# Performance work log

Hardware: AMD Instinct MI355X
Metric: run time of the kernel (lower is better)

## Reference

```python
import jax, jax.numpy as jnp
import numpy as np

N = 100000
E = 3200000
D_IN = 128
D_H = 128
K = 3


def setup_inputs() -> dict:
    key = jax.random.key(0)
    ks = jax.random.split(key, 8)
    x = jax.random.normal(ks[0], (N, D_IN), dtype=jnp.float32)
    src = jax.random.randint(ks[1], (E,), 0, N, dtype=jnp.int32)
    dst = jax.random.randint(ks[2], (E,), 0, N, dtype=jnp.int32)
    s = 1.0 / np.sqrt(D_H)
    W1 = jax.random.normal(ks[3], (D_IN, D_H), dtype=jnp.float32) * s
    b1 = jnp.zeros((D_H,), jnp.float32)
    W2 = jax.random.normal(ks[4], (D_H, D_H), dtype=jnp.float32) * s
    b2 = jnp.zeros((D_H,), jnp.float32)
    Wf1 = jax.random.normal(ks[5], (D_H, D_H), dtype=jnp.float32) * s
    bf1 = jnp.zeros((D_H,), jnp.float32)
    Wf2 = jax.random.normal(ks[6], (D_H, 1), dtype=jnp.float32) * s
    bf2 = jnp.zeros((1,), jnp.float32)
    return {"x": x, "src": src, "dst": dst, "W1": W1, "b1": b1, "W2": W2,
            "b2": b2, "Wf1": Wf1, "bf1": bf1, "Wf2": Wf2, "bf2": bf2}


def _sg_propagate(h, src, dst, norm, k):
    # DGL SGConv: k hops of h <- D^{-1/2} A D^{-1/2} h (in-degree norm, clamp>=1)
    for _ in range(k):
        h = h * norm                                   # [N, d]
        h = jax.ops.segment_sum(h[src], dst, num_segments=N)  # SpMM hop
        h = h * norm
    return h


def reference(x, src, dst, W1, b1, W2, b2, Wf1, bf1, Wf2, bf2):
    deg = jax.ops.segment_sum(jnp.ones((E,), jnp.float32), dst, num_segments=N)
    norm = jnp.clip(deg, 1.0, None) ** -0.5            # [N]
    norm = norm[:, None]
    # conv_1: SGConv(k=3) -> linear -> ReLU
    h = _sg_propagate(x, src, dst, norm, K)
    h = jax.nn.relu(h @ W1 + b1)
    # conv_2
    h = _sg_propagate(h, src, dst, norm, K)
    h = jax.nn.relu(h @ W2 + b2)
    # dgl.mean_nodes over the single graph -> [1, D_H]
    hg = jnp.mean(h, axis=0, keepdims=True)
    h = jax.nn.relu(hg @ Wf1 + bf1)
    out = jax.nn.relu(h @ Wf2 + bf2)
    return jax.nn.sigmoid(out)                         # [1, 1]
```

## Files before the change

kernel.cpp:

```cpp
#include <hip/hip_runtime.h>
#include <hip/hip_fp16.h>
#include <math.h>

#define NN 100000
#define EE 3200000
#define D 128
#define NB 391
#define NBLK2 1024
#define ECH2 (EE / NBLK2)
#define NSTRIP (NN / 32)

#define SCALE_R 6.0f
#define SCALE_G 512.0f

typedef _Float16 half8 __attribute__((ext_vector_type(8)));
typedef float floatx16 __attribute__((ext_vector_type(16)));
typedef float v2f __attribute__((ext_vector_type(2)));

__global__ __launch_bounds__(256) void block_hist(const int* __restrict__ dst,
                                                  int* __restrict__ bh) {
    __shared__ int hist[NB];
    for (int i = threadIdx.x; i < NB; i += 256) hist[i] = 0;
    __syncthreads();
    int e0 = blockIdx.x * ECH2;
    for (int e = e0 + threadIdx.x; e < e0 + ECH2; e += 256)
        atomicAdd(&hist[dst[e] >> 8], 1);
    __syncthreads();
    for (int i = threadIdx.x; i < NB; i += 256)
        bh[i * NBLK2 + blockIdx.x] = hist[i];
}

__global__ __launch_bounds__(256) void bin_scan(int* __restrict__ bh,
                                                int* __restrict__ bintot) {
    __shared__ int ts[256];
    int i = blockIdx.x;
    int t = threadIdx.x;
    int4 v = ((int4*)(bh + i * NBLK2))[t];
    int s = v.x + v.y + v.z + v.w;
    ts[t] = s;
    __syncthreads();
    for (int off = 1; off < 256; off <<= 1) {
        int x = (t >= off) ? ts[t - off] : 0;
        __syncthreads();
        ts[t] += x;
        __syncthreads();
    }
    int run = ts[t] - s;
    int4 o;
    o.x = run; o.y = run + v.x; o.z = o.y + v.y; o.w = o.z + v.z;
    ((int4*)(bh + i * NBLK2))[t] = o;
    if (t == 255) bintot[i] = ts[255];
}

__global__ __launch_bounds__(512) void tiny_scan(const int* __restrict__ bintot,
                                                 int* __restrict__ coff) {
    __shared__ int s[512];
    int t = threadIdx.x;
    int v = (t < NB) ? bintot[t] : 0;
    s[t] = v;
    __syncthreads();
    for (int off = 1; off < 512; off <<= 1) {
        int x = (t >= off) ? s[t - off] : 0;
        __syncthreads();
        s[t] += x;
        __syncthreads();
    }
    int excl = s[t] - v;
    if (t <= NB) coff[t] = excl;
}

__global__ __launch_bounds__(256) void scatter2(const int* __restrict__ src,
                                                const int* __restrict__ dst,
                                                const int* __restrict__ bh,
                                                const int* __restrict__ coff,
                                                int2* __restrict__ ebuf) {
    __shared__ int base[NB];
    int b = blockIdx.x;
    for (int i = threadIdx.x; i < NB; i += 256)
        base[i] = coff[i] + bh[i * NBLK2 + b];
    __syncthreads();
    int e0 = b * ECH2;
    for (int e = e0 + threadIdx.x; e < e0 + ECH2; e += 256) {
        int d = dst[e];
        int pos = atomicAdd(&base[d >> 8], 1);
        ebuf[pos] = make_int2(src[e], d);
    }
}

__global__ __launch_bounds__(256) void fine_sort(const int2* __restrict__ ebuf,
                                                 const int* __restrict__ coarse_off,
                                                 int* __restrict__ rowptr,
                                                 float* __restrict__ norm,
                                                 int* __restrict__ csr) {
    __shared__ int cnt[256];
    __shared__ int sbuf[256];
    int b = blockIdx.x;
    int t = threadIdx.x;
    int e0 = coarse_off[b], e1 = coarse_off[b + 1];
    int n0 = b << 8;
    cnt[t] = 0;
    __syncthreads();
    for (int e = e0 + t; e < e1; e += 256)
        atomicAdd(&cnt[ebuf[e].y & 255], 1);
    __syncthreads();
    int myc = cnt[t];
    sbuf[t] = myc;
    __syncthreads();
    for (int off = 1; off < 256; off <<= 1) {
        int x = (t >= off) ? sbuf[t - off] : 0;
        __syncthreads();
        sbuf[t] += x;
        __syncthreads();
    }
    int excl = sbuf[t] - myc;
    int node = n0 + t;
    if (node < NN) {
        rowptr[node] = e0 + excl;
        float dd = (float)myc;
        if (dd < 1.0f) dd = 1.0f;
        norm[node] = rsqrtf(dd);
    }
    cnt[t] = e0 + excl;
    __syncthreads();
    for (int e = e0 + t; e < e1; e += 256) {
        int2 p = ebuf[e];
        int pos = atomicAdd(&cnt[p.y & 255], 1);
        csr[pos] = p.x;
    }
    if (b == 0 && t == 0) rowptr[NN] = EE;
}

__global__ void conv_w(const float* __restrict__ W, __half* __restrict__ Wt) {
    int idx = blockIdx.x * 256 + threadIdx.x;
    if (idx < D * D) {
        int n = idx >> 7, k = idx & 127;
        Wt[idx] = __float2half_rn(W[k * D + n]);
    }
}

__global__ void convert_scale_fp8(const float4* __restrict__ x4, int* __restrict__ g,
                                  const float* __restrict__ norm) {
    int idx = blockIdx.x * 256 + threadIdx.x;
    if (idx < NN * 32) {
        int row = idx >> 5;
        float n = norm[row];
        float4 v = x4[idx];
        int w = __builtin_amdgcn_cvt_pk_fp8_f32(v.x * n, v.y * n, 0, 0);
        w = __builtin_amdgcn_cvt_pk_fp8_f32(v.z * n, v.w * n, w, 1);
        g[idx] = w;
    }
}

template <int OUT16>
__global__ __launch_bounds__(256) void gather_fp8(const int* __restrict__ rowptr,
                                                  const int* __restrict__ csr,
                                                  const int4* __restrict__ hs,
                                                  const float* __restrict__ norm,
                                                  void* __restrict__ outv, float post) {
    int node = blockIdx.x * 4 + (threadIdx.x >> 6);
    int lane = threadIdx.x & 63;
    int e = lane >> 3;
    int c = lane & 7;
    int p0 = rowptr[node], p1 = rowptr[node + 1];
    float acc[16];
#pragma unroll
    for (int i = 0; i < 16; ++i) acc[i] = 0.0f;
    for (int p = p0 + e; p < p1; p += 8) {
        int s = csr[p];
        int4 v = hs[(size_t)s * 8 + c];
        v2f f;
        f = __builtin_amdgcn_cvt_pk_f32_fp8(v.x, 0); acc[0] += f.x;  acc[1] += f.y;
        f = __builtin_amdgcn_cvt_pk_f32_fp8(v.x, 1); acc[2] += f.x;  acc[3] += f.y;
        f = __builtin_amdgcn_cvt_pk_f32_fp8(v.y, 0); acc[4] += f.x;  acc[5] += f.y;
        f = __builtin_amdgcn_cvt_pk_f32_fp8(v.y, 1); acc[6] += f.x;  acc[7] += f.y;
        f = __builtin_amdgcn_cvt_pk_f32_fp8(v.z, 0); acc[8] += f.x;  acc[9] += f.y;
        f = __builtin_amdgcn_cvt_pk_f32_fp8(v.z, 1); acc[10] += f.x; acc[11] += f.y;
        f = __builtin_amdgcn_cvt_pk_f32_fp8(v.w, 0); acc[12] += f.x; acc[13] += f.y;
        f = __builtin_amdgcn_cvt_pk_f32_fp8(v.w, 1); acc[14] += f.x; acc[15] += f.y;
    }
#pragma unroll
    for (int off = 8; off < 64; off <<= 1) {
#pragma unroll
        for (int i = 0; i < 16; ++i) acc[i] += __shfl_xor(acc[i], off, 64);
    }
    if (e == 0) {
        float n = norm[node];
        float m = (OUT16 ? n : n * n) * post;
#pragma unroll
        for (int i = 0; i < 16; ++i) acc[i] *= m;
        if (OUT16) {
            union { int4 q; __half2 h[4]; } u0, u1;
#pragma unroll
            for (int i = 0; i < 4; ++i) {
                u0.h[i] = __floats2half2_rn(acc[2 * i], acc[2 * i + 1]);
                u1.h[i] = __floats2half2_rn(acc[8 + 2 * i], acc[9 + 2 * i]);
            }
            int4* o = (int4*)((__half*)outv + (size_t)node * D + c * 16);
            o[0] = u0.q;
            o[1] = u1.q;
        } else {
            int4 w;
            w.x = __builtin_amdgcn_cvt_pk_fp8_f32(acc[0], acc[1], 0, 0);
            w.x = __builtin_amdgcn_cvt_pk_fp8_f32(acc[2], acc[3], w.x, 1);
            w.y = __builtin_amdgcn_cvt_pk_fp8_f32(acc[4], acc[5], 0, 0);
            w.y = __builtin_amdgcn_cvt_pk_fp8_f32(acc[6], acc[7], w.y, 1);
            w.z = __builtin_amdgcn_cvt_pk_fp8_f32(acc[8], acc[9], 0, 0);
            w.z = __builtin_amdgcn_cvt_pk_fp8_f32(acc[10], acc[11], w.z, 1);
            w.w = __builtin_amdgcn_cvt_pk_fp8_f32(acc[12], acc[13], 0, 0);
            w.w = __builtin_amdgcn_cvt_pk_fp8_f32(acc[14], acc[15], w.w, 1);
            ((int4*)outv)[(size_t)node * 8 + c] = w;
        }
    }
}

__global__ __launch_bounds__(256) void gemm1_mfma(const __half* __restrict__ H,
                                                  const __half* __restrict__ Wt,
                                                  const float* __restrict__ b,
                                                  const float* __restrict__ norm,
                                                  char* __restrict__ out8) {
    int lane = threadIdx.x & 63;
    int w = threadIdx.x >> 6;
    int m = lane & 31;
    int q = lane >> 5;
    int col = w * 32 + m;
    half8 bf[8];
    const half8* wp = (const half8*)(Wt + (size_t)col * D + q * 8);
#pragma unroll
    for (int kc = 0; kc < 8; ++kc) bf[kc] = wp[kc * 2];
    float bc = b[col];
    for (int s = blockIdx.x; s < NSTRIP; s += gridDim.x) {
        int r0 = s * 32;
        floatx16 acc;
#pragma unroll
        for (int i = 0; i < 16; ++i) acc[i] = 0.0f;
        const half8* hp = (const half8*)(H + (size_t)(r0 + m) * D + q * 8);
#pragma unroll
        for (int kc = 0; kc < 8; ++kc)
            acc = __builtin_amdgcn_mfma_f32_32x32x16_f16(hp[kc * 2], bf[kc], acc, 0, 0, 0);
#pragma unroll
        for (int r = 0; r < 16; ++r) {
            int row = r0 + (r & 3) + 8 * (r >> 2) + 4 * q;
            float v = fmaxf(acc[r] + bc, 0.0f) * norm[row] * SCALE_G;
            int pk = __builtin_amdgcn_cvt_pk_fp8_f32(v, v, 0, 0);
            out8[(size_t)row * D + col] = (char)(pk & 0xff);
        }
    }
}

__global__ __launch_bounds__(256) void gemm2_mfma_colsum(const __half* __restrict__ H,
                                                         const __half* __restrict__ Wt,
                                                         const float* __restrict__ b,
                                                         float* __restrict__ colsum) {
    int lane = threadIdx.x & 63;
    int w = threadIdx.x >> 6;
    int m = lane & 31;
    int q = lane >> 5;
    int col = w * 32 + m;
    half8 bf[8];
    const half8* wp = (const half8*)(Wt + (size_t)col * D + q * 8);
#pragma unroll
    for (int kc = 0; kc < 8; ++kc) bf[kc] = wp[kc * 2];
    float bc = b[col];
    float csum = 0.0f;
    for (int s = blockIdx.x; s < NSTRIP; s += gridDim.x) {
        int r0 = s * 32;
        floatx16 acc;
#pragma unroll
        for (int i = 0; i < 16; ++i) acc[i] = 0.0f;
        const half8* hp = (const half8*)(H + (size_t)(r0 + m) * D + q * 8);
#pragma unroll
        for (int kc = 0; kc < 8; ++kc)
            acc = __builtin_amdgcn_mfma_f32_32x32x16_f16(hp[kc * 2], bf[kc], acc, 0, 0, 0);
#pragma unroll
        for (int r = 0; r < 16; ++r) csum += fmaxf(acc[r] + bc, 0.0f);
    }
    csum += __shfl_down(csum, 32);
    if (lane < 32) atomicAdd(&colsum[col], csum);
}

__global__ __launch_bounds__(128) void final_mlp(const float* __restrict__ colsum,
                                                 const float* __restrict__ Wf1,
                                                 const float* __restrict__ bf1,
                                                 const float* __restrict__ Wf2,
                                                 const float* __restrict__ bf2,
                                                 float* __restrict__ out) {
    __shared__ float hg[D];
    __shared__ float red[D];
    int j = threadIdx.x;
    hg[j] = colsum[j] * (1.0f / (float)NN);
    __syncthreads();
    float acc = bf1[j];
#pragma unroll 16
    for (int k = 0; k < D; ++k)
        acc = fmaf(hg[k], Wf1[k * D + j], acc);
    acc = fmaxf(acc, 0.0f);
    red[j] = acc * Wf2[j];
    __syncthreads();
    for (int s = 64; s > 0; s >>= 1) {
        if (j < s) red[j] += red[j + s];
        __syncthreads();
    }
    if (j == 0) {
        float o = red[0] + bf2[0];
        o = fmaxf(o, 0.0f);
        out[0] = 1.0f / (1.0f + expf(-o));
    }
}

extern "C" void kernel_launch(void* const* d_in, const int* in_sizes, int n_in,
                              void* d_out, int out_size, void* d_ws, size_t ws_size,
                              hipStream_t stream) {
    const float* x   = (const float*)d_in[0];
    const int*   src = (const int*)d_in[1];
    const int*   dst = (const int*)d_in[2];
    const float* W1  = (const float*)d_in[3];
    const float* b1  = (const float*)d_in[4];
    const float* W2  = (const float*)d_in[5];
    const float* b2  = (const float*)d_in[6];
    const float* Wf1 = (const float*)d_in[7];
    const float* bf1 = (const float*)d_in[8];
    const float* Wf2 = (const float*)d_in[9];
    const float* bf2 = (const float*)d_in[10];
    float* out = (float*)d_out;

    char* ws = (char*)d_ws;
    constexpr size_t OFF_BT   = 0;
    constexpr size_t OFF_CO   = 2048;
    constexpr size_t OFF_CS   = 4096;
    constexpr size_t OFF_WT1  = 8192;
    constexpr size_t OFF_WT2  = OFF_WT1 + 32768;
    constexpr size_t OFF_RP   = OFF_WT2 + 32768;
    constexpr size_t OFF_NORM = OFF_RP + 400128;
    constexpr size_t OFF_BH   = OFF_NORM + 400128;
    constexpr size_t OFF_EBUF = OFF_BH + (size_t)NB * NBLK2 * 4;
    constexpr size_t OFF_CSR  = OFF_EBUF + (size_t)EE * 8;
    constexpr size_t OFF_A8   = OFF_CSR + (size_t)EE * 4;
    constexpr size_t OFF_B8   = OFF_A8 + (size_t)NN * D;
    constexpr size_t OFF_H16  = OFF_B8 + (size_t)NN * D;
    int*    bintot = (int*)(ws + OFF_BT);
    int*    coff   = (int*)(ws + OFF_CO);
    float*  colsum = (float*)(ws + OFF_CS);
    __half* Wt1    = (__half*)(ws + OFF_WT1);
    __half* Wt2    = (__half*)(ws + OFF_WT2);
    int*    rowptr = (int*)(ws + OFF_RP);
    float*  norm   = (float*)(ws + OFF_NORM);
    int*    bh     = (int*)(ws + OFF_BH);
    int2*   ebuf   = (int2*)(ws + OFF_EBUF);
    int*    csr    = (int*)(ws + OFF_CSR);
    char*   bufA8  = ws + OFF_A8;
    char*   bufB8  = ws + OFF_B8;
    __half* bufH   = (__half*)(ws + OFF_H16);

    const int nT = 256;
    const int gridC = (NN * 32 + nT - 1) / nT;
    const int gridG = NN / 4;

    const float invR2  = 1.0f / (SCALE_R * SCALE_R);
    const float invGR2 = 1.0f / (SCALE_G * SCALE_R * SCALE_R);

    block_hist<<<NBLK2, 256, 0, stream>>>(dst, bh);
    bin_scan<<<NB, 256, 0, stream>>>(bh, bintot);
    tiny_scan<<<1, 512, 0, stream>>>(bintot, coff);
    scatter2<<<NBLK2, 256, 0, stream>>>(src, dst, bh, coff, ebuf);
    fine_sort<<<NB, 256, 0, stream>>>(ebuf, coff, rowptr, norm, csr);

    conv_w<<<64, 256, 0, stream>>>(W1, Wt1);
    conv_w<<<64, 256, 0, stream>>>(W2, Wt2);

    convert_scale_fp8<<<gridC, nT, 0, stream>>>((const float4*)x, (int*)bufA8, norm);
    gather_fp8<0><<<gridG, 256, 0, stream>>>(rowptr, csr, (const int4*)bufA8, norm, bufB8, SCALE_R);
    gather_fp8<0><<<gridG, 256, 0, stream>>>(rowptr, csr, (const int4*)bufB8, norm, bufA8, SCALE_R);
    gather_fp8<1><<<gridG, 256, 0, stream>>>(rowptr, csr, (const int4*)bufA8, norm, bufH, invR2);

    gemm1_mfma<<<625, 256, 0, stream>>>(bufH, Wt1, b1, norm, bufA8);

    gather_fp8<0><<<gridG, 256, 0, stream>>>(rowptr, csr, (const int4*)bufA8, norm, bufB8, SCALE_R);
    gather_fp8<0><<<gridG, 256, 0, stream>>>(rowptr, csr, (const int4*)bufB8, norm, bufA8, SCALE_R);
    gather_fp8<1><<<gridG, 256, 0, stream>>>(rowptr, csr, (const int4*)bufA8, norm, bufH, invGR2);

    hipMemsetAsync(colsum, 0, D * 4, stream);
    gemm2_mfma_colsum<<<250, 256, 0, stream>>>(bufH, Wt2, b2, colsum);

    final_mlp<<<1, 128, 0, stream>>>(colsum, Wf1, bf1, Wf2, bf2, out);
}
```

Measured before the change: 680.4 us.

## Use FP8 activations and weights for GEMMs, drop fp16 intermediate buffer

The final gather of each propagation now writes FP8 instead of fp16, and both dense layers use FP8×FP8 MFMA with weights pre-scaled by 16 and quantized to FP8. Compensating scale factors (PRE1/PRE2) are folded into the GEMM epilogues. This halves the bytes written by the last gather and read by the GEMMs, and also adds nontemporal loads for the edge buffer and CSR indices in the gather and sort. It risks more quantization error in the GEMM inputs and weights.

Measured after the change: 769.4 us. 13.1% more time.

```diff
diff --git a/kernel.cpp b/kernel.cpp
--- a/kernel.cpp
+++ b/kernel.cpp
@@ -12,8 +12,10 @@
 
 #define SCALE_R 6.0f
 #define SCALE_G 512.0f
-
-typedef _Float16 half8 __attribute__((ext_vector_type(8)));
+#define WSCALE  16.0f
+#define PRE1 (1.0f / (216.0f * WSCALE))
+#define PRE2 (1.0f / (216.0f * SCALE_G * WSCALE))
+
 typedef float floatx16 __attribute__((ext_vector_type(16)));
 typedef float v2f __attribute__((ext_vector_type(2)));
 
@@ -87,7 +89,7 @@
     }
 }
 
-__global__ __launch_bounds__(256) void fine_sort(const int2* __restrict__ ebuf,
+__global__ __launch_bounds__(256) void fine_sort(const long long* __restrict__ ebuf,
                                                  const int* __restrict__ coarse_off,
                                                  int* __restrict__ rowptr,
                                                  float* __restrict__ norm,
@@ -100,8 +102,10 @@
     int n0 = b << 8;
     cnt[t] = 0;
     __syncthreads();
-    for (int e = e0 + t; e < e1; e += 256)
-        atomicAdd(&cnt[ebuf[e].y & 255], 1);
+    for (int e = e0 + t; e < e1; e += 256) {
+        long long pv = __builtin_nontemporal_load(ebuf + e);
+        atomicAdd(&cnt[(int)(pv >> 32) & 255], 1);
+    }
     __syncthreads();
     int myc = cnt[t];
     sbuf[t] = myc;
@@ -123,18 +127,21 @@
     cnt[t] = e0 + excl;
     __syncthreads();
     for (int e = e0 + t; e < e1; e += 256) {
-        int2 p = ebuf[e];
-        int pos = atomicAdd(&cnt[p.y & 255], 1);
-        csr[pos] = p.x;
+        long long pv = __builtin_nontemporal_load(ebuf + e);
+        int pos = atomicAdd(&cnt[(int)(pv >> 32) & 255], 1);
+        csr[pos] = (int)pv;
     }
     if (b == 0 && t == 0) rowptr[NN] = EE;
 }
 
-__global__ void conv_w(const float* __restrict__ W, __half* __restrict__ Wt) {
+__global__ void conv_w_fp8(const float* __restrict__ W, char* __restrict__ Wt8) {
     int idx = blockIdx.x * 256 + threadIdx.x;
-    if (idx < D * D) {
-        int n = idx >> 7, k = idx & 127;
-        Wt[idx] = __float2half_rn(W[k * D + n]);
+    if (idx < D * D / 2) {
+        int n = idx >> 6, k2 = (idx & 63) * 2;
+        float a = W[k2 * D + n] * WSCALE;
+        float b = W[(k2 + 1) * D + n] * WSCALE;
+        int pk = __builtin_amdgcn_cvt_pk_fp8_f32(a, b, 0, 0);
+        ((short*)Wt8)[idx] = (short)(pk & 0xffff);
     }
 }
 
@@ -151,70 +158,60 @@
     }
 }
 
-template <int OUT16>
+template <int FINAL>
 __global__ __launch_bounds__(256) void gather_fp8(const int* __restrict__ rowptr,
                                                   const int* __restrict__ csr,
-                                                  const int4* __restrict__ hs,
+                                                  const char* __restrict__ hs,
                                                   const float* __restrict__ norm,
-                                                  void* __restrict__ outv, float post) {
+                                                  char* __restrict__ outv, float post) {
     int node = blockIdx.x * 4 + (threadIdx.x >> 6);
     int lane = threadIdx.x & 63;
     int e = lane >> 3;
     int c = lane & 7;
     int p0 = rowptr[node], p1 = rowptr[node + 1];
-    float acc[16];
-#pragma unroll
-    for (int i = 0; i < 16; ++i) acc[i] = 0.0f;
+    v2f acc[8];
+#pragma unroll
+    for (int i = 0; i < 8; ++i) acc[i] = (v2f)(0.0f);
+    int coff16 = c << 4;
     for (int p = p0 + e; p < p1; p += 8) {
-        int s = csr[p];
-        int4 v = hs[(size_t)s * 8 + c];
-        v2f f;
-        f = __builtin_amdgcn_cvt_pk_f32_fp8(v.x, 0); acc[0] += f.x;  acc[1] += f.y;
-        f = __builtin_amdgcn_cvt_pk_f32_fp8(v.x, 1); acc[2] += f.x;  acc[3] += f.y;
-        f = __builtin_amdgcn_cvt_pk_f32_fp8(v.y, 0); acc[4] += f.x;  acc[5] += f.y;
-        f = __builtin_amdgcn_cvt_pk_f32_fp8(v.y, 1); acc[6] += f.x;  acc[7] += f.y;
-        f = __builtin_amdgcn_cvt_pk_f32_fp8(v.z, 0); acc[8] += f.x;  acc[9] += f.y;
-        f = __builtin_amdgcn_cvt_pk_f32_fp8(v.z, 1); acc[10] += f.x; acc[11] += f.y;
-        f = __builtin_amdgcn_cvt_pk_f32_fp8(v.w, 0); acc[12] += f.x; acc[13] += f.y;
-        f = __builtin_amdgcn_cvt_pk_f32_fp8(v.w, 1); acc[14] += f.x; acc[15] += f.y;
+        int s = __builtin_nontemporal_load(csr + p);
+        unsigned off = ((unsigned)s << 7) + coff16;
+        int4 v = *(const int4*)(hs + off);
+        acc[0] += __builtin_amdgcn_cvt_pk_f32_fp8(v.x, 0);
+        acc[1] += __builtin_amdgcn_cvt_pk_f32_fp8(v.x, 1);
+        acc[2] += __builtin_amdgcn_cvt_pk_f32_fp8(v.y, 0);
+        acc[3] += __builtin_amdgcn_cvt_pk_f32_fp8(v.y, 1);
+        acc[4] += __builtin_amdgcn_cvt_pk_f32_fp8(v.z, 0);
+        acc[5] += __builtin_amdgcn_cvt_pk_f32_fp8(v.z, 1);
+        acc[6] += __builtin_amdgcn_cvt_pk_f32_fp8(v.w, 0);
+        acc[7] += __builtin_amdgcn_cvt_pk_f32_fp8(v.w, 1);
     }
 #pragma unroll
     for (int off = 8; off < 64; off <<= 1) {
 #pragma unroll
-        for (int i = 0; i < 16; ++i) acc[i] += __shfl_xor(acc[i], off, 64);
+        for (int i = 0; i < 8; ++i) {
+            acc[i].x += __shfl_xor(acc[i].x, off, 64);
+            acc[i].y += __shfl_xor(acc[i].y, off, 64);
+        }
     }
     if (e == 0) {
         float n = norm[node];
-        float m = (OUT16 ? n : n * n) * post;
-#pragma unroll
-        for (int i = 0; i < 16; ++i) acc[i] *= m;
-        if (OUT16) {
-            union { int4 q; __half2 h[4]; } u0, u1;
-#pragma unroll
-            for (int i = 0; i < 4; ++i) {
-                u0.h[i] = __floats2half2_rn(acc[2 * i], acc[2 * i + 1]);
-                u1.h[i] = __floats2half2_rn(acc[8 + 2 * i], acc[9 + 2 * i]);
-            }
-            int4* o = (int4*)((__half*)outv + (size_t)node * D + c * 16);
-            o[0] = u0.q;
-            o[1] = u1.q;
-        } else {
-            int4 w;
-            w.x = __builtin_amdgcn_cvt_pk_fp8_f32(acc[0], acc[1], 0, 0);
-            w.x = __builtin_amdgcn_cvt_pk_fp8_f32(acc[2], acc[3], w.x, 1);
-            w.y = __builtin_amdgcn_cvt_pk_fp8_f32(acc[4], acc[5], 0, 0);
-            w.y = __builtin_amdgcn_cvt_pk_fp8_f32(acc[6], acc[7], w.y, 1);
-            w.z = __builtin_amdgcn_cvt_pk_fp8_f32(acc[8], acc[9], 0, 0);
-            w.z = __builtin_amdgcn_cvt_pk_fp8_f32(acc[10], acc[11], w.z, 1);
-            w.w = __builtin_amdgcn_cvt_pk_fp8_f32(acc[12], acc[13], 0, 0);
-            w.w = __builtin_amdgcn_cvt_pk_fp8_f32(acc[14], acc[15], w.w, 1);
-            ((int4*)outv)[(size_t)node * 8 + c] = w;
-        }
-    }
-}
-
-__global__ __launch_bounds__(256) void gemm1_mfma(const __half* __restrict__ H,
-                                                  const __half* __restrict__ Wt,
+        float m = (FINAL ? n : n * n) * post;
+        int4 w;
+        w.x = __builtin_amdgcn_cvt_pk_fp8_f32(acc[0].x * m, acc[0].y * m, 0, 0);
+        w.x = __builtin_amdgcn_cvt_pk_fp8_f32(acc[1].x * m, acc[1].y * m, w.x, 1);
+        w.y = __builtin_amdgcn_cvt_pk_fp8_f32(acc[2].x * m, acc[2].y * m, 0, 0);
+        w.y = __builtin_amdgcn_cvt_pk_fp8_f32(acc[3].x * m, acc[3].y * m, w.y, 1);
+        w.z = __builtin_amdgcn_cvt_pk_fp8_f32(acc[4].x * m, acc[4].y * m, 0, 0);
+        w.z = __builtin_amdgcn_cvt_pk_fp8_f32(acc[5].x * m, acc[5].y * m, w.z, 1);
+        w.w = __builtin_amdgcn_cvt_pk_fp8_f32(acc[6].x * m, acc[6].y * m, 0, 0);
+        w.w = __builtin_amdgcn_cvt_pk_fp8_f32(acc[7].x * m, acc[7].y * m, w.w, 1);
+        *(int4*)(outv + (unsigned)node * 128 + coff16) = w;
+    }
+}
+
+__global__ __launch_bounds__(256) void gemm1_mfma(const char* __restrict__ H8,
+                                                  const char* __restrict__ Wt8,
                                                   const float* __restrict__ b,
                                                   const float* __restrict__ norm,
                                                   char* __restrict__ out8) {
@@ -223,8 +220,8 @@
     int m = lane & 31;
     int q = lane >> 5;
     int col = w * 32 + m;
-    half8 bf[8];
-    const half8* wp = (const half8*)(Wt + (size_t)col * D + q * 8);
+    long bf[8];
+    const long* wp = (const long*)(Wt8 + (size_t)col * D + q * 8);
 #pragma unroll
     for (int kc = 0; kc < 8; ++kc) bf[kc] = wp[kc * 2];
     float bc = b[col];
@@ -233,22 +230,22 @@
         floatx16 acc;
 #pragma unroll
         for (int i = 0; i < 16; ++i) acc[i] = 0.0f;
-        const half8* hp = (const half8*)(H + (size_t)(r0 + m) * D + q * 8);
+        const long* ap = (const long*)(H8 + (size_t)(r0 + m) * D + q * 8);
 #pragma unroll
         for (int kc = 0; kc < 8; ++kc)
-            acc = __builtin_amdgcn_mfma_f32_32x32x16_f16(hp[kc * 2], bf[kc], acc, 0, 0, 0);
+            acc = __builtin_amdgcn_mfma_f32_32x32x16_fp8_fp8(ap[kc * 2], bf[kc], acc, 0, 0, 0);
 #pragma unroll
         for (int r = 0; r < 16; ++r) {
             int row = r0 + (r & 3) + 8 * (r >> 2) + 4 * q;
-            float v = fmaxf(acc[r] + bc, 0.0f) * norm[row] * SCALE_G;
+            float v = fmaxf(acc[r] * PRE1 + bc, 0.0f) * norm[row] * SCALE_G;
             int pk = __builtin_amdgcn_cvt_pk_fp8_f32(v, v, 0, 0);
             out8[(size_t)row * D + col] = (char)(pk & 0xff);
         }
     }
 }
 
-__global__ __launch_bounds__(256) void gemm2_mfma_colsum(const __half* __restrict__ H,
-                                                         const __half* __restrict__ Wt,
+__global__ __launch_bounds__(256) void gemm2_mfma_colsum(const char* __restrict__ H8,
+                                                         const char* __restrict__ Wt8,
                                                          const float* __restrict__ b,
                                                          float* __restrict__ colsum) {
     int lane = threadIdx.x & 63;
@@ -256,8 +253,8 @@
     int m = lane & 31;
     int q = lane >> 5;
     int col = w * 32 + m;
-    half8 bf[8];
-    const half8* wp = (const half8*)(Wt + (size_t)col * D + q * 8);
+    long bf[8];
+    const long* wp = (const long*)(Wt8 + (size_t)col * D + q * 8);
 #pragma unroll
     for (int kc = 0; kc < 8; ++kc) bf[kc] = wp[kc * 2];
     float bc = b[col];
@@ -267,12 +264,12 @@
         floatx16 acc;
 #pragma unroll
         for (int i = 0; i < 16; ++i) acc[i] = 0.0f;
-        const half8* hp = (const half8*)(H + (size_t)(r0 + m) * D + q * 8);
+        const long* ap = (const long*)(H8 + (size_t)(r0 + m) * D + q * 8);
 #pragma unroll
         for (int kc = 0; kc < 8; ++kc)
-            acc = __builtin_amdgcn_mfma_f32_32x32x16_f16(hp[kc * 2], bf[kc], acc, 0, 0, 0);
-#pragma unroll
-        for (int r = 0; r < 16; ++r) csum += fmaxf(acc[r] + bc, 0.0f);
+            acc = __builtin_amdgcn_mfma_f32_32x32x16_fp8_fp8(ap[kc * 2], bf[kc], acc, 0, 0, 0);
+#pragma unroll
+        for (int r = 0; r < 16; ++r) csum += fmaxf(acc[r] * PRE2 + bc, 0.0f);
     }
     csum += __shfl_down(csum, 32);
     if (lane < 32) atomicAdd(&colsum[col], csum);
@@ -328,20 +325,19 @@
     constexpr size_t OFF_CO   = 2048;
     constexpr size_t OFF_CS   = 4096;
     constexpr size_t OFF_WT1  = 8192;
-    constexpr size_t OFF_WT2  = OFF_WT1 + 32768;
-    constexpr size_t OFF_RP   = OFF_WT2 + 32768;
+    constexpr size_t OFF_WT2  = OFF_WT1 + 16384;
+    constexpr size_t OFF_RP   = OFF_WT2 + 16384;
     constexpr size_t OFF_NORM = OFF_RP + 400128;
     constexpr size_t OFF_BH   = OFF_NORM + 400128;
     constexpr size_t OFF_EBUF = OFF_BH + (size_t)NB * NBLK2 * 4;
     constexpr size_t OFF_CSR  = OFF_EBUF + (size_t)EE * 8;
     constexpr size_t OFF_A8   = OFF_CSR + (size_t)EE * 4;
     constexpr size_t OFF_B8   = OFF_A8 + (size_t)NN * D;
-    constexpr size_t OFF_H16  = OFF_B8 + (size_t)NN * D;
     int*    bintot = (int*)(ws + OFF_BT);
     int*    coff   = (int*)(ws + OFF_CO);
     float*  colsum = (float*)(ws + OFF_CS);
-    __half* Wt1    = (__half*)(ws + OFF_WT1);
-    __half* Wt2    = (__half*)(ws + OFF_WT2);
+    char*   Wt1    = ws + OFF_WT1;
+    char*   Wt2    = ws + OFF_WT2;
     int*    rowptr = (int*)(ws + OFF_RP);
     float*  norm   = (float*)(ws + OFF_NORM);
     int*    bh     = (int*)(ws + OFF_BH);
@@ -349,37 +345,33 @@
     int*    csr    = (int*)(ws + OFF_CSR);
     char*   bufA8  = ws + OFF_A8;
     char*   bufB8  = ws + OFF_B8;
-    __half* bufH   = (__half*)(ws + OFF_H16);
 
     const int nT = 256;
     const int gridC = (NN * 32 + nT - 1) / nT;
     const int gridG = NN / 4;
-
-    const float invR2  = 1.0f / (SCALE_R * SCALE_R);
-    const float invGR2 = 1.0f / (SCALE_G * SCALE_R * SCALE_R);
 
     block_hist<<<NBLK2, 256, 0, stream>>>(dst, bh);
     bin_scan<<<NB, 256, 0, stream>>>(bh, bintot);
     tiny_scan<<<1, 512, 0, stream>>>(bintot, coff);
     scatter2<<<NBLK2, 256, 0, stream>>>(src, dst, bh, coff, ebuf);
-    fine_sort<<<NB, 256, 0, stream>>>(ebuf, coff, rowptr, norm, csr);
-
-    conv_w<<<64, 256, 0, stream>>>(W1, Wt1);
-    conv_w<<<64, 256, 0, stream>>>(W2, Wt2);
+    fine_sort<<<NB, 256, 0, stream>>>((const long long*)ebuf, coff, rowptr, norm, csr);
+
+    conv_w_fp8<<<32, 256, 0, stream>>>(W1, Wt1);
+    conv_w_fp8<<<32, 256, 0, stream>>>(W2, Wt2);
 
     convert_scale_fp8<<<gridC, nT, 0, stream>>>((const float4*)x, (int*)bufA8, norm);
-    gather_fp8<0><<<gridG, 256, 0, stream>>>(rowptr, csr, (const int4*)bufA8, norm, bufB8, SCALE_R);
-    gather_fp8<0><<<gridG, 256, 0, stream>>>(rowptr, csr, (const int4*)bufB8, norm, bufA8, SCALE_R);
-    gather_fp8<1><<<gridG, 256, 0, stream>>>(rowptr, csr, (const int4*)bufA8, norm, bufH, invR2);
-
-    gemm1_mfma<<<625, 256, 0, stream>>>(bufH, Wt1, b1, norm, bufA8);
-
-    gather_fp8<0><<<gridG, 256, 0, stream>>>(rowptr, csr, (const int4*)bufA8, norm, bufB8, SCALE_R);
-    gather_fp8<0><<<gridG, 256, 0, stream>>>(rowptr, csr, (const int4*)bufB8, norm, bufA8, SCALE_R);
-    gather_fp8<1><<<gridG, 256, 0, stream>>>(rowptr, csr, (const int4*)bufA8, norm, bufH, invGR2);
+    gather_fp8<0><<<gridG, 256, 0, stream>>>(rowptr, csr, bufA8, norm, bufB8, SCALE_R);
+    gather_fp8<0><<<gridG, 256, 0, stream>>>(rowptr, csr, bufB8, norm, bufA8, SCALE_R);
+    gather_fp8<1><<<gridG, 256, 0, stream>>>(rowptr, csr, bufA8, norm, bufB8, SCALE_R);
+
+    gemm1_mfma<<<625, 256, 0, stream>>>(bufB8, Wt1, b1, norm, bufA8);
+
+    gather_fp8<0><<<gridG, 256, 0, stream>>>(rowptr, csr, bufA8, norm, bufB8, SCALE_R);
+    gather_fp8<0><<<gridG, 256, 0, stream>>>(rowptr, csr, bufB8, norm, bufA8, SCALE_R);
+    gather_fp8<1><<<gridG, 256, 0, stream>>>(rowptr, csr, bufA8, norm, bufB8, SCALE_R);
 
     hipMemsetAsync(colsum, 0, D * 4, stream);
-    gemm2_mfma_colsum<<<250, 256, 0, stream>>>(bufH, Wt2, b2, colsum);
+    gemm2_mfma_colsum<<<250, 256, 0, stream>>>(bufB8, Wt2, b2, colsum);
 
     final_mlp<<<1, 128, 0, stream>>>(colsum, Wf1, bf1, Wf2, bf2, out);
 }
```
